# Kernel optimization log

Measured on AMD Instinct MI355X. Metric: run time of the kernel, lower is better.

## Reference

```python
import jax, jax.numpy as jnp
import numpy as np


def _selective_scan(u, delta, A, Bm, Cm, Dskip, delta_bias):
    # u, delta: (B, K*D, L); A: (K*D, N); Bm, Cm: (B, K, N, L); Dskip, delta_bias: (K*D,)
    Bsz, KD, L = u.shape
    K = Bm.shape[1]
    D = KD // K
    N = A.shape[1]
    dt = jax.nn.softplus(delta + delta_bias[None, :, None])          # (B,KD,L)
    u4 = u.reshape(Bsz, K, D, L)
    dt4 = dt.reshape(Bsz, K, D, L)
    A4 = A.reshape(K, D, N)
    # discretization: dA = exp(dt*A), dBu = dt * B * u
    dA = jnp.exp(dt4[..., None] * A4[None, :, :, None, :])            # (B,K,D,L,N)
    Bt = jnp.transpose(Bm, (0, 1, 3, 2))                               # (B,K,L,N)
    dBu = dt4[..., None] * u4[..., None] * Bt[:, :, None, :, :]        # (B,K,D,L,N)
    dA_l = jnp.moveaxis(dA, 3, 0)                                      # (L,B,K,D,N)
    dBu_l = jnp.moveaxis(dBu, 3, 0)

    def step(h, ab):
        a, b = ab
        h = a * h + b
        return h, h

    h0 = jnp.zeros(dA_l.shape[1:], dA.dtype)
    _, hs = jax.lax.scan(step, h0, (dA_l, dBu_l))                      # (L,B,K,D,N)
    C_l = jnp.moveaxis(Cm, 3, 0)                                       # (L,B,K,N)
    y = jnp.einsum('lbkdn,lbkn->lbkd', hs, C_l)                        # (L,B,K,D)
    y = jnp.moveaxis(y, 0, 3).reshape(Bsz, KD, L)
    return y + u * Dskip[None, :, None]


def setup_inputs() -> dict:
    key = jax.random.key(0)
    ks = jax.random.split(key, 8)
    B, H, W, C = 2, 64, 64, 96
    Di, N, K = 192, 16, 4
    R = 6  # ceil(96/16)
    x = jax.random.normal(ks[0], (B, H, W, C), jnp.float32)
    in_proj_w = jax.random.normal(ks[1], (2 * Di, C), jnp.float32) * (C ** -0.5)
    conv_w = jax.random.normal(ks[2], (Di, 1, 3, 3), jnp.float32) * 0.2
    conv_b = jax.random.normal(ks[3], (Di,), jnp.float32) * 0.02
    x_proj_weight = jax.random.normal(ks[4], (K, R + 2 * N, Di), jnp.float32) * (Di ** -0.5)
    dt_projs_weight = jax.random.uniform(ks[5], (K, Di, R), jnp.float32, -(R ** -0.5), R ** -0.5)
    dt = jnp.exp(jax.random.uniform(ks[6], (K, Di), jnp.float32) * (np.log(0.1) - np.log(0.001)) + np.log(0.001))
    dt = jnp.clip(dt, 1e-4)
    dt_projs_bias = dt + jnp.log(-jnp.expm1(-dt))                      # inverse softplus
    A_logs = jnp.log(jnp.tile(jnp.arange(1, N + 1, dtype=jnp.float32), (K * Di, 1)))
    Ds = jnp.ones((K * Di,), jnp.float32)
    out_norm_w = jnp.ones((Di,), jnp.float32)
    out_norm_b = jnp.zeros((Di,), jnp.float32)
    out_proj_w = jax.random.normal(ks[7], (C, Di), jnp.float32) * (Di ** -0.5)
    return dict(x=x, in_proj_w=in_proj_w, conv_w=conv_w, conv_b=conv_b,
                x_proj_weight=x_proj_weight, dt_projs_weight=dt_projs_weight,
                dt_projs_bias=dt_projs_bias, A_logs=A_logs, Ds=Ds,
                out_norm_w=out_norm_w, out_norm_b=out_norm_b, out_proj_w=out_proj_w)


def reference(x, in_proj_w, conv_w, conv_b, x_proj_weight, dt_projs_weight,
              dt_projs_bias, A_logs, Ds, out_norm_w, out_norm_b, out_proj_w):
    Bsz, H, W, C = x.shape
    Di = conv_w.shape[0]
    K = x_proj_weight.shape[0]
    R = dt_projs_weight.shape[2]
    N = A_logs.shape[1]
    L = H * W
    # in_proj (bias=False) and split into x, z
    xz = x @ in_proj_w.T                                               # (B,H,W,2*Di)
    xi, z = jnp.split(xz, 2, axis=-1)
    # depthwise conv2d + SiLU (channel-first)
    xc = jnp.transpose(xi, (0, 3, 1, 2))                               # (B,Di,H,W)
    xc = jax.lax.conv_general_dilated(xc, conv_w, (1, 1), 'SAME',
                                      feature_group_count=Di) + conv_b[None, :, None, None]
    xc = jax.nn.silu(xc)
    # cross-scan: 4 directions (row-major, col-major, and their reverses)
    x0 = xc.reshape(Bsz, Di, L)
    x1 = jnp.transpose(xc, (0, 1, 3, 2)).reshape(Bsz, Di, L)
    xs = jnp.stack([x0, x1, x0[..., ::-1], x1[..., ::-1]], axis=1)      # (B,K,Di,L)
    # per-direction projections
    x_dbl = jnp.einsum('bkdl,kcd->bkcl', xs, x_proj_weight)            # (B,K,R+2N,L)
    dts, Bs, Cs = jnp.split(x_dbl, [R, R + N], axis=2)
    dts = jnp.einsum('bkrl,kdr->bkdl', dts, dt_projs_weight)           # (B,K,Di,L)
    A = -jnp.exp(A_logs)                                               # (K*Di,N)
    ys = _selective_scan(xs.reshape(Bsz, K * Di, L), dts.reshape(Bsz, K * Di, L),
                         A, Bs, Cs, Ds, dt_projs_bias.reshape(-1))
    ys = ys.reshape(Bsz, K, Di, L)
    # cross-merge
    y = ys[:, 0] + ys[:, 2, :, ::-1]
    yt = ys[:, 1] + ys[:, 3, :, ::-1]                                  # col-major ordering
    y = y + jnp.transpose(yt.reshape(Bsz, Di, W, H), (0, 1, 3, 2)).reshape(Bsz, Di, L)
    y = jnp.transpose(y.reshape(Bsz, Di, H, W), (0, 2, 3, 1))          # (B,H,W,Di)
    # out_norm: LayerNorm over channel
    mu = jnp.mean(y, axis=-1, keepdims=True)
    var = jnp.mean((y - mu) ** 2, axis=-1, keepdims=True)
    y = (y - mu) * jax.lax.rsqrt(var + 1e-5) * out_norm_w + out_norm_b
    # gate and out_proj (bias=False)
    y = y * jax.nn.silu(z)
    return y @ out_proj_w.T
```

## Files before the change

kernel.cpp:

```cpp
#include <hip/hip_runtime.h>
#include <hip/hip_fp16.h>
#include <math.h>


static constexpr int Bsz = 2;
static constexpr int Lc  = 4096;
static constexpr int Cc  = 96;
static constexpr int Dd  = 192;
static constexpr int Kk  = 4;
static constexpr int NC  = 32;

__device__ __forceinline__ float bu(unsigned short v) {
    return __uint_as_float((unsigned int)v << 16);
}
__device__ __forceinline__ unsigned short f2b(float f) {
    unsigned int u = __float_as_uint(f);
    return (unsigned short)((u + 0x7fffu + ((u >> 16) & 1u)) >> 16);
}

template<int CTRL>
__device__ __forceinline__ float dppadd(float x) {
    return x + __int_as_float(__builtin_amdgcn_update_dpp(
        0, __float_as_int(x), CTRL, 0xf, 0xf, true));
}
__device__ __forceinline__ float red16(float x) {
    x = dppadd<0xB1>(x);
    x = dppadd<0x4E>(x);
    x = dppadd<0x124>(x);
    x = dppadd<0x128>(x);
    return x;
}

__global__ __launch_bounds__(256) void k0_detect(const unsigned short* __restrict__ x,
                                                 int* __restrict__ flag)
{
    __shared__ int s[256];
    int cnt = 0;
    for (int i = threadIdx.x; i < 4096; i += 256) {
        int e = (x[i] >> 7) & 0xFF;
        cnt += (e >= 118 && e <= 131) ? 1 : 0;
    }
    s[threadIdx.x] = cnt;
    __syncthreads();
    for (int st = 128; st > 0; st >>= 1) {
        if (threadIdx.x < st) s[threadIdx.x] += s[threadIdx.x + st];
        __syncthreads();
    }
    if (threadIdx.x == 0) flag[0] = (s[0] >= 3072) ? 1 : 0;
}

struct Cv {
    const void* src[12];
    int off[12];
    int n[12];
};
__global__ __launch_bounds__(256) void k0b_convert(Cv cv, const int* __restrict__ flag,
                                                   float* __restrict__ dstbase)
{
    int bf = flag[0];
    int t = blockIdx.y;
    int i = blockIdx.x * 256 + threadIdx.x;
    if (i >= cv.n[t]) return;
    if (t == 11) {
        int cp = i % 40;
        int d  = (i / 40) % 192;
        int k  = i / 7680;
        float v = 0.f;
        if (cp < 38) {
            size_t si = (size_t)(k * 38 + cp) * 192 + d;
            v = bf ? bu(((const unsigned short*)cv.src[11])[si])
                   : ((const float*)cv.src[11])[si];
        }
        dstbase[cv.off[11] + i] = v;
        return;
    }
    float v;
    if (bf) v = bu(((const unsigned short*)cv.src[t])[i]);
    else    v = ((const float*)cv.src[t])[i];
    dstbase[cv.off[t] + i] = v;
}

__global__ __launch_bounds__(256) void k1_inproj(const void* __restrict__ xraw,
                                                 const int* __restrict__ flag,
                                                 const float* __restrict__ wf,
                                                 float* __restrict__ xiT, __half* __restrict__ zT)
{
    __shared__ float xT[64 * 97];
    const int bf = flag[0];
    int lt = blockIdx.x & 127;
    int jq = blockIdx.x >> 7;
    int row0 = lt * 64;
    for (int e = threadIdx.x; e < 64 * 96; e += 256) {
        int i = e / 96, c = e % 96;
        size_t idx = (size_t)(row0 + i) * Cc + c;
        xT[i * 97 + c] = bf ? bu(((const unsigned short*)xraw)[idx])
                            : ((const float*)xraw)[idx];
    }
    __syncthreads();
    int pi = threadIdx.x & 63;
    int q  = __builtin_amdgcn_readfirstlane(threadIdx.x >> 6);
    int j0 = jq * 96 + q * 24;
    float acc[24];
#pragma unroll
    for (int j = 0; j < 24; ++j) acc[j] = 0.f;
    for (int c4 = 0; c4 < 24; ++c4) {
        float xv0 = xT[pi * 97 + c4 * 4 + 0];
        float xv1 = xT[pi * 97 + c4 * 4 + 1];
        float xv2 = xT[pi * 97 + c4 * 4 + 2];
        float xv3 = xT[pi * 97 + c4 * 4 + 3];
#pragma unroll
        for (int j = 0; j < 24; ++j) {
            float4 w4 = *reinterpret_cast<const float4*>(&wf[(size_t)(j0 + j) * 96 + c4 * 4]);
            acc[j] += w4.x * xv0 + w4.y * xv1 + w4.z * xv2 + w4.w * xv3;
        }
    }
    int b = row0 >> 12;
    int l = (row0 & 4095) + pi;
    if (jq < 2) {
#pragma unroll
        for (int j = 0; j < 24; ++j)
            xiT[((size_t)b * Dd + j0 + j) * Lc + l] = acc[j];
    } else {
#pragma unroll
        for (int j = 0; j < 24; ++j) {
            float v = acc[j];
            zT[((size_t)b * Dd + (j0 + j - 192)) * Lc + l] =
                __float2half(v / (1.f + __expf(-v)));
        }
    }
}

__global__ __launch_bounds__(256) void k2b_conv(const float* __restrict__ xiT,
                                                const float* __restrict__ cwf,
                                                const float* __restrict__ cbf,
                                                float* __restrict__ xc,
                                                float* __restrict__ uT)
{
    __shared__ float inl[34 * 66];
    __shared__ float outl[32 * 65];
    int bid = blockIdx.x;
    int half = bid & 1;
    int d = (bid >> 1) % Dd;
    int b = bid / (2 * Dd);
    int h0 = half * 32;
    const float* src = xiT + (size_t)(b * Dd + d) * Lc;
    for (int r = threadIdx.x; r < 34; r += 256) {
        inl[r * 66 + 0] = 0.f;
        inl[r * 66 + 65] = 0.f;
    }
    for (int e = threadIdx.x; e < 34 * 64; e += 256) {
        int row = e >> 6, w = e & 63;
        int h = h0 - 1 + row;
        inl[row * 66 + 1 + w] = (h >= 0 && h < 64) ? src[h * 64 + w] : 0.f;
    }
    __syncthreads();
    float wgt[9];
#pragma unroll
    for (int t = 0; t < 9; t++) wgt[t] = cwf[d * 9 + t];
    float bias = cbf[d];
    int hs = threadIdx.x >> 6, w = threadIdx.x & 63;
    float* dstrow = xc + (size_t)(b * Dd + d) * Lc;
#pragma unroll
    for (int it = 0; it < 8; ++it) {
        int hh = it * 4 + hs;
        float acc = bias;
#pragma unroll
        for (int dy = 0; dy < 3; ++dy) {
            const float* rp = &inl[(hh + dy) * 66 + w];
#pragma unroll
            for (int dx = 0; dx < 3; ++dx)
                acc += rp[dx] * wgt[dy * 3 + dx];
        }
        float s = acc / (1.f + __expf(-acc));
        dstrow[(h0 + hh) * 64 + w] = s;
        outl[hh * 65 + w] = s;
    }
    __syncthreads();
    float* udst = uT + (size_t)(b * Dd + d) * Lc;
    for (int e = threadIdx.x; e < 2048; e += 256) {
        int w2 = e >> 5, hh2 = e & 31;
        udst[w2 * 64 + h0 + hh2] = outl[hh2 * 65 + w2];
    }
}

__global__ __launch_bounds__(256) void k3_proj(const float* __restrict__ xc,
                                               const float* __restrict__ uT,
                                               const float* __restrict__ Wg,
                                               const float* __restrict__ dtwf,
                                               const float* __restrict__ dtbf,
                                               __half* __restrict__ dtH,
                                               float* __restrict__ BsT, float* __restrict__ CsT)
{
    __shared__ float xL[192 * 64];
    __shared__ float rawdt[6][64];
    int bid = blockIdx.x;
    int pt = bid & 63, k = (bid >> 6) & 3, b = bid >> 8;
    int s0 = pt * 64;
    const float* xb = ((k & 1) ? uT : xc) + (size_t)b * Dd * Lc + s0;
    for (int e = threadIdx.x; e < 3072; e += 256) {
        int d = e >> 4, c4 = e & 15;
        *reinterpret_cast<float4*>(&xL[d * 64 + c4 * 4]) =
            *reinterpret_cast<const float4*>(xb + (size_t)d * Lc + c4 * 4);
    }
    __syncthreads();

    int pi = threadIdx.x & 63;
    int q  = __builtin_amdgcn_readfirstlane(threadIdx.x >> 6);

    const float* wk = Wg + (size_t)k * 192 * 40 + q * 10;

    float acc[10];
#pragma unroll
    for (int j = 0; j < 10; ++j) acc[j] = 0.f;

    for (int d = 0; d < 192; ++d) {
        float xv = xL[d * 64 + pi];
        const float* wrow = wk + d * 40;
#pragma unroll
        for (int j = 0; j < 10; ++j) acc[j] += wrow[j] * xv;
    }

    if (q == 0) {
#pragma unroll
        for (int j = 0; j < 6; ++j) rawdt[j][pi] = acc[j];
    }
    size_t bk16 = (size_t)(b * Kk + k) * 16;
#pragma unroll
    for (int j = 0; j < 10; ++j) {
        int cp = q * 10 + j;
        if (cp >= 6 && cp < 22)
            BsT[(bk16 + (cp - 6)) * Lc + s0 + pi] = acc[j];
        else if (cp >= 22 && cp < 38)
            CsT[(bk16 + (cp - 22)) * Lc + s0 + pi] = acc[j];
    }
    __syncthreads();

    float raws[6];
#pragma unroll
    for (int r = 0; r < 6; ++r) raws[r] = rawdt[r][pi];
    const float* dtw = dtwf + (size_t)(k * 192 + q * 48) * 6;
    const float* dtb = dtbf + k * 192 + q * 48;
    __half* dto = dtH + ((size_t)(b * Kk + k) * Dd + q * 48) * Lc + s0 + pi;
    for (int dd = 0; dd < 48; ++dd) {
        float s = dtb[dd];
#pragma unroll
        for (int r = 0; r < 6; ++r) s += raws[r] * dtw[dd * 6 + r];
        float sp = fmaxf(s, 0.f) + __logf(1.f + __expf(-fabsf(s)));
        dto[(size_t)dd * Lc] = __float2half(sp);
    }
}

template<int REV, int PASS3>
__device__ __forceinline__ void scan_run(const float* __restrict__ ubase,
                                         const __half* __restrict__ dbase,
                                         const float* __restrict__ Bbase,
                                         const float* __restrict__ Cbase,
                                         float* uL, float* bL, float* cL, __half* dL,
                                         int dl, int n, int c,
                                         float An,
                                         float* __restrict__ P, float* __restrict__ S,
                                         size_t pidx, __half* __restrict__ yrow)
{
    const int t0 = c * 128;
    const int tg = REV ? (Lc - 128 - t0) : t0;

    {
        float4 ru0 = *reinterpret_cast<const float4*>(ubase + tg + n * 4);
        float4 ru1 = *reinterpret_cast<const float4*>(ubase + tg + 64 + n * 4);
        float4 rb0 = *reinterpret_cast<const float4*>(Bbase + tg + n * 4);
        float4 rb1 = *reinterpret_cast<const float4*>(Bbase + tg + 64 + n * 4);
        uint4  rd  = *reinterpret_cast<const uint4*>(dbase + tg + n * 8);
        *reinterpret_cast<float4*>(uL + dl * 132 + n * 4) = ru0;
        *reinterpret_cast<float4*>(uL + dl * 132 + 64 + n * 4) = ru1;
        *reinterpret_cast<float4*>(bL + dl * 132 + n * 4) = rb0;
        *reinterpret_cast<float4*>(bL + dl * 132 + 64 + n * 4) = rb1;
        *reinterpret_cast<uint4*>(dL + dl * 136 + n * 8) = rd;
        if (PASS3) {
            float4 rc0 = *reinterpret_cast<const float4*>(Cbase + tg + n * 4);
            float4 rc1 = *reinterpret_cast<const float4*>(Cbase + tg + 64 + n * 4);
            *reinterpret_cast<float4*>(cL + dl * 132 + n * 4) = rc0;
            *reinterpret_cast<float4*>(cL + dl * 132 + 64 + n * 4) = rc1;
        }
    }
    __syncthreads();

    float h = PASS3 ? P[pidx] : 0.f;
    float sdt = 0.f, ystash = 0.f;

#pragma unroll 4
    for (int qi = 0; qi < 32; ++qi) {
        const int col4 = REV ? (124 - qi * 4) : (qi * 4);
        float4 uq = *reinterpret_cast<const float4*>(uL + dl * 132 + col4);
        float4 bq = *reinterpret_cast<const float4*>(bL + n * 132 + col4);
        float4 cq{};
        if (PASS3) cq = *reinterpret_cast<const float4*>(cL + n * 132 + col4);
        uint2 dq = *reinterpret_cast<const uint2*>(dL + dl * 136 + col4);
        const __half2* dh2 = reinterpret_cast<const __half2*>(&dq);
#pragma unroll
        for (int j = 0; j < 4; ++j) {
            const int e = REV ? (3 - j) : j;
            float dtv = (e & 1) ? __high2float(dh2[e >> 1]) : __low2float(dh2[e >> 1]);
            float uv = reinterpret_cast<const float*>(&uq)[e];
            float bv = reinterpret_cast<const float*>(&bq)[e];
            float a = __expf(dtv * An);
            if (!PASS3) sdt += dtv;
            h = a * h + (dtv * uv) * bv;
            if (PASS3) {
                float cv = reinterpret_cast<const float*>(&cq)[e];
                float yv = red16(h * cv);
                const int i15 = (qi & 3) * 4 + j;
                if (i15 == n) ystash = yv;
                if (i15 == 15) {
                    int tb = t0 + (qi >> 2) * 16 + n;
                    int aw = REV ? (Lc - 1 - tb) : tb;
                    yrow[aw] = __float2half(ystash);
                }
            }
        }
    }

    if (!PASS3) {
        P[pidx] = __expf(An * sdt);
        S[pidx] = h;
    }
}

template<int PASS3>
__global__ __launch_bounds__(256) void kscan(const __half* __restrict__ dtH,
                                             const float* __restrict__ xc,
                                             const float* __restrict__ uT,
                                             const float* __restrict__ BsT,
                                             const float* __restrict__ CsT,
                                             const float* __restrict__ alogf,
                                             float* __restrict__ P,
                                             float* __restrict__ S,
                                             __half* __restrict__ ysH)
{
    __shared__ float uL[16 * 132];
    __shared__ float bL[16 * 132];
    __shared__ float cL[PASS3 ? 16 * 132 : 4];
    __shared__ __half dL[16 * 136];

    int c  = blockIdx.x & 31;
    int t1 = blockIdx.x >> 5;
    int dg = t1 % 12;
    int kk = (t1 / 12) & 3;
    int b  = t1 / 48;
    int n  = threadIdx.x & 15, dl = threadIdx.x >> 4;
    int d  = dg * 16 + dl;

    const float* ubz = ((kk & 1) ? uT : xc) + (size_t)b * Dd * Lc;
    const float*  ubase = ubz + (size_t)d * Lc;
    const __half* dbase = dtH + ((size_t)((b * Kk + kk) * Dd + d)) * Lc;
    const float*  Bbase = BsT + ((size_t)((b * Kk + kk) * 16 + dl)) * Lc;
    const float*  Cbase = CsT + ((size_t)((b * Kk + kk) * 16 + dl)) * Lc;

    float An  = -__expf(alogf[(kk * Dd + d) * 16 + n]);
    size_t pidx = (((size_t)(b * Kk + kk) * Dd + d) * NC + c) * 16 + n;
    __half* yrow = PASS3 ? ysH + ((size_t)(kk * Bsz + b) * Dd + d) * Lc : nullptr;

    if (kk >= 2)
        scan_run<1, PASS3>(ubase, dbase, Bbase, Cbase, uL, bL, cL, dL,
                           dl, n, c, An, P, S, pidx, yrow);
    else
        scan_run<0, PASS3>(ubase, dbase, Bbase, Cbase, uL, bL, cL, dL,
                           dl, n, c, An, P, S, pidx, yrow);
}

__global__ __launch_bounds__(64) void k6_pass2(float* __restrict__ P, const float* __restrict__ S)
{
    int g = blockIdx.x * 64 + threadIdx.x;
    int n = g & 15;
    int chain = g >> 4;
    size_t base = (size_t)chain * NC * 16 + n;
    float h = 0.f;
#pragma unroll
    for (int c = 0; c < NC; ++c) {
        size_t id = base + (size_t)c * 16;
        float p = P[id], s = S[id];
        P[id] = h;
        h = p * h + s;
    }
}

__global__ __launch_bounds__(256) void k8t(const __half* __restrict__ ysH,
                                           __half* __restrict__ ysT)
{
    __shared__ float t[64 * 65];
    int bid = blockIdx.x;
    int d = bid % Dd, b = bid / Dd;
    const __half* y1 = ysH + ((size_t)(1 * Bsz + b) * Dd + d) * Lc;
    const __half* y3 = ysH + ((size_t)(3 * Bsz + b) * Dd + d) * Lc;
    __half* dst = ysT + ((size_t)b * Dd + d) * Lc;
    for (int e = threadIdx.x; e < 4096; e += 256)
        t[(e >> 6) * 65 + (e & 63)] = __half2float(y1[e]) + __half2float(y3[e]);
    __syncthreads();
    for (int e = threadIdx.x; e < 4096; e += 256)
        dst[e] = __float2half(t[(e & 63) * 65 + (e >> 6)]);
}

__global__ __launch_bounds__(256) void k8_norm(const __half* __restrict__ ysH,
                                               const __half* __restrict__ ysT,
                                               const __half* __restrict__ zT,
                                               const float* __restrict__ xc,
                                               const float* __restrict__ dsf,
                                               const float* __restrict__ nwf,
                                               const float* __restrict__ nbf,
                                               __half* __restrict__ gH)
{
    __shared__ float yt[192 * 33];
    __shared__ float ps1[8 * 32], ps2[8 * 32];
    __shared__ float mu[32], rs[32];
    int bid = blockIdx.x;
    int pt = bid & 127, b = bid >> 7;
    int p0 = pt * 32;
    for (int e = threadIdx.x; e < 192 * 32; e += 256) {
        int d = e >> 5, p = e & 31;
        size_t r0 = ((size_t)(0 * Bsz + b) * Dd + d) * Lc + p0 + p;
        size_t r2 = ((size_t)(2 * Bsz + b) * Dd + d) * Lc + p0 + p;
        size_t rt = ((size_t)b * Dd + d) * Lc + p0 + p;
        float ds4 = dsf[d] + dsf[192 + d] + dsf[384 + d] + dsf[576 + d];
        yt[d * 33 + p] = __half2float(ysH[r0]) + __half2float(ysH[r2])
                       + __half2float(ysT[rt])
                       + xc[((size_t)b * Dd + d) * Lc + p0 + p] * ds4;
    }
    __syncthreads();
    {
        int p = threadIdx.x & 31, q = threadIdx.x >> 5;
        float s1 = 0.f, s2 = 0.f;
        for (int dd = 0; dd < 24; ++dd) {
            float v = yt[(q * 24 + dd) * 33 + p];
            s1 += v; s2 += v * v;
        }
        ps1[q * 32 + p] = s1; ps2[q * 32 + p] = s2;
    }
    __syncthreads();
    if (threadIdx.x < 32) {
        int p = threadIdx.x;
        float s1 = 0.f, s2 = 0.f;
        for (int q = 0; q < 8; ++q) { s1 += ps1[q * 32 + p]; s2 += ps2[q * 32 + p]; }
        float m = s1 * (1.f / 192.f);
        float var = s2 * (1.f / 192.f) - m * m;
        mu[p] = m; rs[p] = rsqrtf(var + 1e-5f);
    }
    __syncthreads();
    for (int e = threadIdx.x; e < 192 * 32; e += 256) {
        int d = e >> 5, p = e & 31;
        float v = (yt[d * 33 + p] - mu[p]) * rs[p] * nwf[d] + nbf[d];
        float zv = __half2float(zT[((size_t)b * Dd + d) * Lc + p0 + p]);
        yt[d * 33 + p] = v * zv;
    }
    __syncthreads();
    for (int i = threadIdx.x; i < 32 * 192; i += 256) {
        int p = i / 192, d = i - p * 192;
        gH[((size_t)b * Lc + p0 + p) * Dd + d] = __float2half(yt[d * 33 + p]);
    }
}

__global__ __launch_bounds__(256) void k10_outproj(const __half* __restrict__ gH,
                                                   const float* __restrict__ wof,
                                                   const int* __restrict__ flag,
                                                   void* __restrict__ outv)
{
    __shared__ float wT[192 * 100];
    const int bf = flag[0];
    for (int e = threadIdx.x; e < 96 * 192; e += 256) {
        int cI = e / 192, dI = e - cI * 192;
        wT[dI * 100 + cI] = wof[e];
    }
    __syncthreads();
    int r0 = blockIdx.x * 32;
    int r = threadIdx.x >> 3, cg = threadIdx.x & 7;
    const __half* grow = gH + (size_t)(r0 + r) * Dd;
    float acc[12];
#pragma unroll
    for (int i = 0; i < 12; ++i) acc[i] = 0.f;
    for (int d0 = 0; d0 < 192; d0 += 8) {
        __half2 g2[4];
        *reinterpret_cast<uint4*>(g2) = *reinterpret_cast<const uint4*>(grow + d0);
#pragma unroll
        for (int j = 0; j < 8; ++j) {
            float gf = (j & 1) ? __high2float(g2[j >> 1]) : __low2float(g2[j >> 1]);
            const float* wrow = &wT[(d0 + j) * 100 + cg * 12];
            float4 w0 = *reinterpret_cast<const float4*>(wrow);
            float4 w1 = *reinterpret_cast<const float4*>(wrow + 4);
            float4 w2 = *reinterpret_cast<const float4*>(wrow + 8);
            acc[0] += gf * w0.x; acc[1] += gf * w0.y; acc[2]  += gf * w0.z; acc[3]  += gf * w0.w;
            acc[4] += gf * w1.x; acc[5] += gf * w1.y; acc[6]  += gf * w1.z; acc[7]  += gf * w1.w;
            acc[8] += gf * w2.x; acc[9] += gf * w2.y; acc[10] += gf * w2.z; acc[11] += gf * w2.w;
        }
    }
    size_t obase = (size_t)(r0 + r) * Cc + cg * 12;
    if (bf) {
        unsigned short* o = (unsigned short*)outv;
#pragma unroll
        for (int cc = 0; cc < 12; ++cc) o[obase + cc] = f2b(acc[cc]);
    } else {
        float* o = (float*)outv;
#pragma unroll
        for (int cc = 0; cc < 12; ++cc) o[obase + cc] = acc[cc];
    }
}

extern "C" void kernel_launch(void* const* d_in, const int* in_sizes, int n_in,
                              void* d_out, int out_size, void* d_ws, size_t ws_size,
                              hipStream_t stream)
{
    (void)out_size; (void)ws_size;
    float* ws = (float*)d_ws;
    int* flag = (int*)ws;

    int off[12]; int tot = 64;
    off[0] = 0;
    for (int i = 1; i < 12; ++i) {
        off[i] = tot;
        int n = (i < n_in) ? in_sizes[i] : 0;
        tot += (n + 63) & ~63;
    }
    float* winf = ws + off[1];
    float* cwf  = ws + off[2];
    float* cbf  = ws + off[3];
    float* dtwf = ws + off[5];
    float* dtbf = ws + off[6];
    float* alogf= ws + off[7];
    float* dsf  = ws + off[8];
    float* nwf  = ws + off[9];
    float* nbf  = ws + off[10];
    float* wof  = ws + off[11];

    const size_t BASE = 131072;
    __half* dtH = (__half*)(ws + BASE);
    float*  xc  = ws + BASE + 3145728;
    float*  uT  = ws + BASE + 4718592;
    float*  BsT = ws + BASE + 6291456;
    float*  CsT = ws + BASE + 6815744;
    float*  P   = ws + BASE + 7340032;
    float*  S   = ws + BASE + 8126464;
    __half* zT  = (__half*)(ws + BASE + 8912896);
    float*  xiT = ws + BASE + 9699328;
    __half* ysH = (__half*)(ws + BASE + 9699328);
    __half* ysT = (__half*)P;
    __half* gH  = (__half*)S;
    float*  Wg  = ws + BASE + 12845056;

    Cv cv2;
    for (int i = 0; i < 11; ++i) {
        int t = i + 1;
        cv2.src[i] = (t < n_in) ? d_in[t] : d_in[0];
        cv2.off[i] = off[t];
        cv2.n[i]   = (t < n_in) ? in_sizes[t] : 0;
    }
    cv2.src[11] = (4 < n_in) ? d_in[4] : d_in[0];
    cv2.off[11] = (int)(BASE + 12845056);
    cv2.n[11]   = 4 * 192 * 40;

    k0_detect   <<<dim3(1),    dim3(256), 0, stream>>>((const unsigned short*)d_in[0], flag);
    k0b_convert <<<dim3(144, 12), dim3(256), 0, stream>>>(cv2, flag, ws);
    k1_inproj   <<<dim3(512),  dim3(256), 0, stream>>>(d_in[0], flag, winf, xiT, zT);
    k2b_conv    <<<dim3(768),  dim3(256), 0, stream>>>(xiT, cwf, cbf, xc, uT);
    k3_proj     <<<dim3(512),  dim3(256), 0, stream>>>(xc, uT, Wg, dtwf, dtbf, dtH, BsT, CsT);
    kscan<0>    <<<dim3(3072), dim3(256), 0, stream>>>(dtH, xc, uT, BsT, CsT, alogf, P, S, ysH);
    k6_pass2    <<<dim3(384),  dim3(64),  0, stream>>>(P, S);
    kscan<1>    <<<dim3(3072), dim3(256), 0, stream>>>(dtH, xc, uT, BsT, CsT, alogf, P, S, ysH);
    k8t         <<<dim3(384),  dim3(256), 0, stream>>>(ysH, ysT);
    k8_norm     <<<dim3(256),  dim3(256), 0, stream>>>(ysH, ysT, zT, xc, dsf, nwf, nbf, gH);
    k10_outproj <<<dim3(256),  dim3(256), 0, stream>>>(gH, wof, flag, d_out);
}
```

Measured before the change: 179.9 us.

## Split scan chunk staging into halves with register prefetch; restructure out_proj

The scan kernels now stage each 128-step chunk in two 64-step halves. The second half is loaded into registers while the first half is scanned, then written to shared memory. This halves LDS use per block, which may raise occupancy and hides global load latency behind compute, at the cost of an extra barrier pair. The output projection is also rewritten to 1024-thread blocks that transpose 64 rows of the gated activations into shared memory. Each wave computes 6 output channels, reading weights directly through wave-uniform global loads instead of staging the full weight matrix in LDS per block.

New measurement: 182.5 us. No clear change (+1.5%).

```diff
diff --git a/kernel.cpp b/kernel.cpp
--- a/kernel.cpp
+++ b/kernel.cpp
@@ -262,62 +262,73 @@
                                          size_t pidx, __half* __restrict__ yrow)
 {
     const int t0 = c * 128;
-    const int tg = REV ? (Lc - 128 - t0) : t0;
-
-    {
-        float4 ru0 = *reinterpret_cast<const float4*>(ubase + tg + n * 4);
-        float4 ru1 = *reinterpret_cast<const float4*>(ubase + tg + 64 + n * 4);
-        float4 rb0 = *reinterpret_cast<const float4*>(Bbase + tg + n * 4);
-        float4 rb1 = *reinterpret_cast<const float4*>(Bbase + tg + 64 + n * 4);
-        uint4  rd  = *reinterpret_cast<const uint4*>(dbase + tg + n * 8);
-        *reinterpret_cast<float4*>(uL + dl * 132 + n * 4) = ru0;
-        *reinterpret_cast<float4*>(uL + dl * 132 + 64 + n * 4) = ru1;
-        *reinterpret_cast<float4*>(bL + dl * 132 + n * 4) = rb0;
-        *reinterpret_cast<float4*>(bL + dl * 132 + 64 + n * 4) = rb1;
-        *reinterpret_cast<uint4*>(dL + dl * 136 + n * 8) = rd;
-        if (PASS3) {
-            float4 rc0 = *reinterpret_cast<const float4*>(Cbase + tg + n * 4);
-            float4 rc1 = *reinterpret_cast<const float4*>(Cbase + tg + 64 + n * 4);
-            *reinterpret_cast<float4*>(cL + dl * 132 + n * 4) = rc0;
-            *reinterpret_cast<float4*>(cL + dl * 132 + 64 + n * 4) = rc1;
-        }
-    }
-    __syncthreads();
+    const int mb0 = REV ? (Lc - 64 - t0) : t0;
+    const int mb1 = REV ? (Lc - 128 - t0) : (t0 + 64);
+
+    float4 ru = *reinterpret_cast<const float4*>(ubase + mb0 + n * 4);
+    float4 rb = *reinterpret_cast<const float4*>(Bbase + mb0 + n * 4);
+    float4 rc{};
+    if (PASS3) rc = *reinterpret_cast<const float4*>(Cbase + mb0 + n * 4);
+    uint2 rd = *reinterpret_cast<const uint2*>(dbase + mb0 + n * 4);
+    *reinterpret_cast<float4*>(uL + dl * 68 + n * 4) = ru;
+    *reinterpret_cast<float4*>(bL + dl * 68 + n * 4) = rb;
+    if (PASS3) *reinterpret_cast<float4*>(cL + dl * 68 + n * 4) = rc;
+    *reinterpret_cast<uint2*>(dL + dl * 72 + n * 4) = rd;
+    __syncthreads();
+
+    ru = *reinterpret_cast<const float4*>(ubase + mb1 + n * 4);
+    rb = *reinterpret_cast<const float4*>(Bbase + mb1 + n * 4);
+    if (PASS3) rc = *reinterpret_cast<const float4*>(Cbase + mb1 + n * 4);
+    rd = *reinterpret_cast<const uint2*>(dbase + mb1 + n * 4);
 
     float h = PASS3 ? P[pidx] : 0.f;
     float sdt = 0.f, ystash = 0.f;
 
-#pragma unroll 4
-    for (int qi = 0; qi < 32; ++qi) {
-        const int col4 = REV ? (124 - qi * 4) : (qi * 4);
-        float4 uq = *reinterpret_cast<const float4*>(uL + dl * 132 + col4);
-        float4 bq = *reinterpret_cast<const float4*>(bL + n * 132 + col4);
-        float4 cq{};
-        if (PASS3) cq = *reinterpret_cast<const float4*>(cL + n * 132 + col4);
-        uint2 dq = *reinterpret_cast<const uint2*>(dL + dl * 136 + col4);
-        const __half2* dh2 = reinterpret_cast<const __half2*>(&dq);
-#pragma unroll
-        for (int j = 0; j < 4; ++j) {
-            const int e = REV ? (3 - j) : j;
-            float dtv = (e & 1) ? __high2float(dh2[e >> 1]) : __low2float(dh2[e >> 1]);
-            float uv = reinterpret_cast<const float*>(&uq)[e];
-            float bv = reinterpret_cast<const float*>(&bq)[e];
-            float a = __expf(dtv * An);
-            if (!PASS3) sdt += dtv;
-            h = a * h + (dtv * uv) * bv;
-            if (PASS3) {
-                float cv = reinterpret_cast<const float*>(&cq)[e];
-                float yv = red16(h * cv);
-                const int i15 = (qi & 3) * 4 + j;
-                if (i15 == n) ystash = yv;
-                if (i15 == 15) {
-                    int tb = t0 + (qi >> 2) * 16 + n;
-                    int aw = REV ? (Lc - 1 - tb) : tb;
-                    yrow[aw] = __float2half(ystash);
-                }
-            }
-        }
-    }
+#define SS2D_HALF(HH)                                                           \
+    {                                                                           \
+        _Pragma("unroll 4")                                                     \
+        for (int qi = 0; qi < 16; ++qi) {                                       \
+            const int col4 = REV ? (60 - qi * 4) : (qi * 4);                    \
+            float4 uq = *reinterpret_cast<const float4*>(uL + dl * 68 + col4);  \
+            float4 bq = *reinterpret_cast<const float4*>(bL + n * 68 + col4);   \
+            float4 cq{};                                                        \
+            if (PASS3) cq = *reinterpret_cast<const float4*>(cL + n * 68 + col4);\
+            uint2 dq = *reinterpret_cast<const uint2*>(dL + dl * 72 + col4);    \
+            const __half2* dh2 = reinterpret_cast<const __half2*>(&dq);         \
+            _Pragma("unroll")                                                   \
+            for (int j = 0; j < 4; ++j) {                                       \
+                const int e = REV ? (3 - j) : j;                                \
+                float dtv = (e & 1) ? __high2float(dh2[e >> 1])                 \
+                                    : __low2float(dh2[e >> 1]);                 \
+                float uv = reinterpret_cast<const float*>(&uq)[e];              \
+                float bv = reinterpret_cast<const float*>(&bq)[e];              \
+                float a = __expf(dtv * An);                                     \
+                if (!PASS3) sdt += dtv;                                         \
+                h = a * h + (dtv * uv) * bv;                                    \
+                if (PASS3) {                                                    \
+                    float cv = reinterpret_cast<const float*>(&cq)[e];          \
+                    float yv = red16(h * cv);                                   \
+                    const int i15 = (qi & 3) * 4 + j;                           \
+                    if (i15 == n) ystash = yv;                                  \
+                    if (i15 == 15) {                                            \
+                        int tb = t0 + (HH) * 64 + (qi >> 2) * 16 + n;           \
+                        int aw = REV ? (Lc - 1 - tb) : tb;                      \
+                        yrow[aw] = __float2half(ystash);                        \
+                    }                                                           \
+                }                                                               \
+            }                                                                   \
+        }                                                                       \
+    }
+
+    SS2D_HALF(0);
+    __syncthreads();
+    *reinterpret_cast<float4*>(uL + dl * 68 + n * 4) = ru;
+    *reinterpret_cast<float4*>(bL + dl * 68 + n * 4) = rb;
+    if (PASS3) *reinterpret_cast<float4*>(cL + dl * 68 + n * 4) = rc;
+    *reinterpret_cast<uint2*>(dL + dl * 72 + n * 4) = rd;
+    __syncthreads();
+    SS2D_HALF(1);
+#undef SS2D_HALF
 
     if (!PASS3) {
         P[pidx] = __expf(An * sdt);
@@ -336,10 +347,10 @@
                                              float* __restrict__ S,
                                              __half* __restrict__ ysH)
 {
-    __shared__ float uL[16 * 132];
-    __shared__ float bL[16 * 132];
-    __shared__ float cL[PASS3 ? 16 * 132 : 4];
-    __shared__ __half dL[16 * 136];
+    __shared__ float uL[16 * 68];
+    __shared__ float bL[16 * 68];
+    __shared__ float cL[PASS3 ? 16 * 68 : 4];
+    __shared__ __half dL[16 * 72];
 
     int c  = blockIdx.x & 31;
     int t1 = blockIdx.x >> 5;
@@ -457,48 +468,47 @@
     }
 }
 
-__global__ __launch_bounds__(256) void k10_outproj(const __half* __restrict__ gH,
-                                                   const float* __restrict__ wof,
-                                                   const int* __restrict__ flag,
-                                                   void* __restrict__ outv)
-{
-    __shared__ float wT[192 * 100];
+__global__ __launch_bounds__(1024) void k10_outproj(const __half* __restrict__ gH,
+                                                    const float* __restrict__ wof,
+                                                    const int* __restrict__ flag,
+                                                    void* __restrict__ outv)
+{
+    __shared__ float gLT[192 * 66];
     const int bf = flag[0];
-    for (int e = threadIdx.x; e < 96 * 192; e += 256) {
-        int cI = e / 192, dI = e - cI * 192;
-        wT[dI * 100 + cI] = wof[e];
-    }
-    __syncthreads();
-    int r0 = blockIdx.x * 32;
-    int r = threadIdx.x >> 3, cg = threadIdx.x & 7;
-    const __half* grow = gH + (size_t)(r0 + r) * Dd;
-    float acc[12];
-#pragma unroll
-    for (int i = 0; i < 12; ++i) acc[i] = 0.f;
-    for (int d0 = 0; d0 < 192; d0 += 8) {
+    int r0 = blockIdx.x * 64;
+    for (int e = threadIdx.x; e < 1536; e += 1024) {
+        int row = e / 24, j = e % 24;
         __half2 g2[4];
-        *reinterpret_cast<uint4*>(g2) = *reinterpret_cast<const uint4*>(grow + d0);
-#pragma unroll
-        for (int j = 0; j < 8; ++j) {
-            float gf = (j & 1) ? __high2float(g2[j >> 1]) : __low2float(g2[j >> 1]);
-            const float* wrow = &wT[(d0 + j) * 100 + cg * 12];
-            float4 w0 = *reinterpret_cast<const float4*>(wrow);
-            float4 w1 = *reinterpret_cast<const float4*>(wrow + 4);
-            float4 w2 = *reinterpret_cast<const float4*>(wrow + 8);
-            acc[0] += gf * w0.x; acc[1] += gf * w0.y; acc[2]  += gf * w0.z; acc[3]  += gf * w0.w;
-            acc[4] += gf * w1.x; acc[5] += gf * w1.y; acc[6]  += gf * w1.z; acc[7]  += gf * w1.w;
-            acc[8] += gf * w2.x; acc[9] += gf * w2.y; acc[10] += gf * w2.z; acc[11] += gf * w2.w;
+        *reinterpret_cast<uint4*>(g2) =
+            *reinterpret_cast<const uint4*>(gH + (size_t)(r0 + row) * Dd + j * 8);
+#pragma unroll
+        for (int i = 0; i < 4; ++i) {
+            gLT[(j * 8 + 2 * i + 0) * 66 + row] = __low2float(g2[i]);
+            gLT[(j * 8 + 2 * i + 1) * 66 + row] = __high2float(g2[i]);
         }
     }
-    size_t obase = (size_t)(r0 + r) * Cc + cg * 12;
+    __syncthreads();
+    int row = threadIdx.x & 63;
+    int w = __builtin_amdgcn_readfirstlane(threadIdx.x >> 6);
+    int c0 = w * 6;
+    const float* wr = wof + (size_t)c0 * Dd;
+    float acc[6];
+#pragma unroll
+    for (int i = 0; i < 6; ++i) acc[i] = 0.f;
+    for (int d = 0; d < 192; ++d) {
+        float gv = gLT[d * 66 + row];
+#pragma unroll
+        for (int cc = 0; cc < 6; ++cc) acc[cc] += wr[(size_t)cc * Dd + d] * gv;
+    }
+    size_t ob = (size_t)(r0 + row) * Cc + c0;
     if (bf) {
         unsigned short* o = (unsigned short*)outv;
 #pragma unroll
-        for (int cc = 0; cc < 12; ++cc) o[obase + cc] = f2b(acc[cc]);
+        for (int cc = 0; cc < 6; ++cc) o[ob + cc] = f2b(acc[cc]);
     } else {
         float* o = (float*)outv;
 #pragma unroll
-        for (int cc = 0; cc < 12; ++cc) o[obase + cc] = acc[cc];
+        for (int cc = 0; cc < 6; ++cc) o[ob + cc] = acc[cc];
     }
 }
 
@@ -564,5 +574,5 @@
     kscan<1>    <<<dim3(3072), dim3(256), 0, stream>>>(dtH, xc, uT, BsT, CsT, alogf, P, S, ysH);
     k8t         <<<dim3(384),  dim3(256), 0, stream>>>(ysH, ysT);
     k8_norm     <<<dim3(256),  dim3(256), 0, stream>>>(ysH, ysT, zT, xc, dsf, nwf, nbf, gH);
-    k10_outproj <<<dim3(256),  dim3(256), 0, stream>>>(gH, wof, flag, d_out);
-}
+    k10_outproj <<<dim3(128),  dim3(1024), 0, stream>>>(gH, wof, flag, d_out);
+}
```
